# Optimization experiments

Hardware: AMD Instinct MI355X
Metric: run time of the kernel (lower is better)

The kernel has to match this reference:

```python
import jax, jax.numpy as jnp
import numpy as np

BATCH, SIZE_IN, SIZE_OUT = 2048, 256, 512


def setup_inputs() -> dict:
    key = jax.random.key(0)
    kx, ka = jax.random.split(key)
    x = jax.random.normal(kx, (BATCH, SIZE_IN), dtype=jnp.float32)
    A = jax.random.normal(ka, (SIZE_IN, SIZE_OUT), dtype=jnp.float32)
    return {"x": x, "A": A}


def reference(x, A):
    # W = sigmoid(A): [size_in, size_out]
    W = jax.nn.sigmoid(A)
    # tropical (max-times) matmul: out[i,k] = max_j W[j,k] * x[i,j]
    # broadcast [B,1,J_in->axis1]... x: [B,J,1], W: [1,J,K] -> [B,J,K] -> max over J
    out = jnp.max(x[:, :, None] * W[None, :, :], axis=1)  # [B, K]
    return out
```

## Files before the change

kernel.cpp:

```cpp
#include <hip/hip_runtime.h>


constexpr int JD = 256;
constexpr int KD = 512;
constexpr int TI = 4;
constexpr int ROWS = 16;
constexpr int NCH = 16;

typedef _Float16 h1;
typedef __attribute__((ext_vector_type(2))) _Float16 h2v;
typedef __attribute__((ext_vector_type(4))) float f4;

__device__ __forceinline__ float sigmoidf_fast(float a) {
    return 1.0f / (1.0f + __expf(-a));
}

__global__ __launch_bounds__(256) void wpack(const float* __restrict__ A,
                                             h2v* __restrict__ Wp) {
    const int t  = blockIdx.x * 256 + threadIdx.x;
    const int p  = t >> 7;
    const int kq = (t & 127) << 2;
    const f4 a0 = *(const f4*)&A[(2 * p) * KD + kq];
    const f4 a1 = *(const f4*)&A[(2 * p + 1) * KD + kq];
    union { f4 v; h2v h[4]; } u;
    #pragma unroll
    for (int q = 0; q < 4; ++q)
        u.h[q] = h2v{(h1)sigmoidf_fast(a0[q]), (h1)sigmoidf_fast(a1[q])};
    *(f4*)&Wp[p * KD + kq] = u.v;
}

__global__ __launch_bounds__(256, 4) void tropical_mm_kernel(
        const float* __restrict__ x,
        const h2v* __restrict__ Wp,
        float* __restrict__ out) {
    __shared__ h2v xl[ROWS][JD / 2];

    const int t    = (int)threadIdx.x;
    const int lane = t & 63;
    const int wv   = __builtin_amdgcn_readfirstlane(t >> 6);
    const int bk   = (int)blockIdx.x & 7;
    const int bi   = (int)blockIdx.x >> 3;
    const int i0   = bi * ROWS;
    const int k    = bk * 64 + lane;

    {
        const int srow = t >> 4;
        const int scf  = (t & 15) * 16;
        const float* xs = x + (i0 + srow) * JD + scf;
        f4 f0 = ((const f4*)xs)[0];
        f4 f1 = ((const f4*)xs)[1];
        f4 f2 = ((const f4*)xs)[2];
        f4 f3 = ((const f4*)xs)[3];
        union { f4 v; h2v h[4]; } u0, u1;
        u0.h[0] = h2v{(h1)f0.x, (h1)f0.y};
        u0.h[1] = h2v{(h1)f0.z, (h1)f0.w};
        u0.h[2] = h2v{(h1)f1.x, (h1)f1.y};
        u0.h[3] = h2v{(h1)f1.z, (h1)f1.w};
        u1.h[0] = h2v{(h1)f2.x, (h1)f2.y};
        u1.h[1] = h2v{(h1)f2.z, (h1)f2.w};
        u1.h[2] = h2v{(h1)f3.x, (h1)f3.y};
        u1.h[3] = h2v{(h1)f3.z, (h1)f3.w};
        *(f4*)&xl[srow][(t & 15) * 8]     = u0.v;
        *(f4*)&xl[srow][(t & 15) * 8 + 4] = u1.v;
    }
    __syncthreads();

    const h2v* Wk = Wp + k;
    const int r0 = wv * TI;

    h2v acc[TI];
    #pragma unroll
    for (int r = 0; r < TI; ++r)
        acc[r] = h2v{(h1)(-65504.0f), (h1)(-65504.0f)};

    h2v WA[8], WB[8];
    f4  XA[TI][2], XB[TI][2];

    auto loadW = [&](h2v (&W)[8], int c) {
        const h2v* p = Wk + (c * 8) * KD;
        #pragma unroll
        for (int q = 0; q < 8; ++q) W[q] = p[q * KD];
    };
    auto loadX = [&](f4 (&X)[TI][2], int c) {
        #pragma unroll
        for (int r = 0; r < TI; ++r) {
            X[r][0] = *(const f4*)&xl[r0 + r][c * 8];
            X[r][1] = *(const f4*)&xl[r0 + r][c * 8 + 4];
        }
    };
    auto compute = [&](const f4 (&X)[TI][2], const h2v (&W)[8]) {
        #pragma unroll
        for (int r = 0; r < TI; ++r) {
            #pragma unroll
            for (int hf = 0; hf < 2; ++hf) {
                union { f4 v; h2v h[4]; } u;
                u.v = X[r][hf];
                #pragma unroll
                for (int q = 0; q < 4; ++q)
                    acc[r] = __builtin_elementwise_max(
                        acc[r], u.h[q] * W[hf * 4 + q]);
            }
        }
    };

    loadW(WA, 0);
    loadX(XA, 0);

    #pragma unroll 1
    for (int c = 0; c < NCH; c += 2) {
        loadW(WB, c + 1);
        loadX(XB, c + 1);
        compute(XA, WA);
        if (c + 2 < NCH) {
            loadW(WA, c + 2);
            loadX(XA, c + 2);
        }
        compute(XB, WB);
    }

    #pragma unroll
    for (int r = 0; r < TI; ++r) {
        const float lo = (float)acc[r][0];
        const float hi = (float)acc[r][1];
        out[(i0 + r0 + r) * KD + k] = fmaxf(lo, hi);
    }
}

extern "C" void kernel_launch(void* const* d_in, const int* in_sizes, int n_in,
                              void* d_out, int out_size, void* d_ws, size_t ws_size,
                              hipStream_t stream) {
    const float* x = (const float*)d_in[0];
    const float* A = (const float*)d_in[1];
    float* out = (float*)d_out;
    h2v* Wp = (h2v*)d_ws;

    hipLaunchKernelGGL(wpack, dim3(64), dim3(256), 0, stream, A, Wp);

    hipLaunchKernelGGL(tropical_mm_kernel, dim3(1024), dim3(256), 0, stream,
                       x, Wp, out);
}
```

Measured before the change: 23.57 us.

## Fuse sigmoid packing into tropical matmul with W staged in LDS

```diff
diff --git a/kernel.cpp b/kernel.cpp
--- a/kernel.cpp
+++ b/kernel.cpp
@@ -1,129 +1,136 @@
 #include <hip/hip_runtime.h>
 
-
-constexpr int JD = 256;
-constexpr int KD = 512;
-constexpr int TI = 4;
-constexpr int ROWS = 16;
-constexpr int NCH = 16;
 
 typedef _Float16 h1;
 typedef __attribute__((ext_vector_type(2))) _Float16 h2v;
 typedef __attribute__((ext_vector_type(4))) float f4;
 
+constexpr int JD   = 256;
+constexpr int KD   = 512;
+constexpr int BI   = 32;
+constexpr int KW   = 64;
+constexpr int TI   = 8;
+constexpr int LSTR = 132;
+constexpr int NCH  = 16;
+
 __device__ __forceinline__ float sigmoidf_fast(float a) {
     return 1.0f / (1.0f + __expf(-a));
 }
 
-__global__ __launch_bounds__(256) void wpack(const float* __restrict__ A,
-                                             h2v* __restrict__ Wp) {
-    const int t  = blockIdx.x * 256 + threadIdx.x;
-    const int p  = t >> 7;
-    const int kq = (t & 127) << 2;
-    const f4 a0 = *(const f4*)&A[(2 * p) * KD + kq];
-    const f4 a1 = *(const f4*)&A[(2 * p + 1) * KD + kq];
-    union { f4 v; h2v h[4]; } u;
-    #pragma unroll
-    for (int q = 0; q < 4; ++q)
-        u.h[q] = h2v{(h1)sigmoidf_fast(a0[q]), (h1)sigmoidf_fast(a1[q])};
-    *(f4*)&Wp[p * KD + kq] = u.v;
-}
+__global__ __launch_bounds__(256) void tropical_fused(
+        const float* __restrict__ x,
+        const float* __restrict__ A,
+        float* __restrict__ out) {
+    __shared__ h2v xl[BI * LSTR];
+    __shared__ h2v Wl[KW * LSTR];
 
-__global__ __launch_bounds__(256, 4) void tropical_mm_kernel(
-        const float* __restrict__ x,
-        const h2v* __restrict__ Wp,
-        float* __restrict__ out) {
-    __shared__ h2v xl[ROWS][JD / 2];
-
-    const int t    = (int)threadIdx.x;
-    const int lane = t & 63;
-    const int wv   = __builtin_amdgcn_readfirstlane(t >> 6);
-    const int bk   = (int)blockIdx.x & 7;
-    const int bi   = (int)blockIdx.x >> 3;
-    const int i0   = bi * ROWS;
-    const int k    = bk * 64 + lane;
+    const int t  = (int)threadIdx.x;
+    const int kg = (int)blockIdx.x & 7;
+    const int ib = (int)blockIdx.x >> 3;
+    const int i0 = ib * BI;
+    const int k0 = kg * KW;
 
     {
-        const int srow = t >> 4;
-        const int scf  = (t & 15) * 16;
-        const float* xs = x + (i0 + srow) * JD + scf;
-        f4 f0 = ((const f4*)xs)[0];
-        f4 f1 = ((const f4*)xs)[1];
-        f4 f2 = ((const f4*)xs)[2];
-        f4 f3 = ((const f4*)xs)[3];
-        union { f4 v; h2v h[4]; } u0, u1;
-        u0.h[0] = h2v{(h1)f0.x, (h1)f0.y};
-        u0.h[1] = h2v{(h1)f0.z, (h1)f0.w};
-        u0.h[2] = h2v{(h1)f1.x, (h1)f1.y};
-        u0.h[3] = h2v{(h1)f1.z, (h1)f1.w};
-        u1.h[0] = h2v{(h1)f2.x, (h1)f2.y};
-        u1.h[1] = h2v{(h1)f2.z, (h1)f2.w};
-        u1.h[2] = h2v{(h1)f3.x, (h1)f3.y};
-        u1.h[3] = h2v{(h1)f3.z, (h1)f3.w};
-        *(f4*)&xl[srow][(t & 15) * 8]     = u0.v;
-        *(f4*)&xl[srow][(t & 15) * 8 + 4] = u1.v;
+        const int srow = t >> 3;
+        const int c0   = (t & 7) * 32;
+        const float* xs = x + (i0 + srow) * JD + c0;
+        #pragma unroll
+        for (int q = 0; q < 4; ++q) {
+            const f4 v0 = ((const f4*)xs)[2 * q];
+            const f4 v1 = ((const f4*)xs)[2 * q + 1];
+            union { f4 v; h2v h[4]; } u;
+            u.h[0] = h2v{(h1)v0.x, (h1)v0.y};
+            u.h[1] = h2v{(h1)v0.z, (h1)v0.w};
+            u.h[2] = h2v{(h1)v1.x, (h1)v1.y};
+            u.h[3] = h2v{(h1)v1.z, (h1)v1.w};
+            *(f4*)&xl[srow * LSTR + c0 / 2 + q * 4] = u.v;
+        }
+    }
+
+    {
+        const int kl = t & 63;
+        const int j0 = (t >> 6) * 64;
+        const float* Ak = A + k0 + kl;
+        #pragma unroll 1
+        for (int pass = 0; pass < 4; ++pass) {
+            const int jb = j0 + pass * 16;
+            float s[16];
+            #pragma unroll
+            for (int m = 0; m < 16; ++m)
+                s[m] = Ak[(jb + m) * KD];
+            union { f4 v; h2v h[4]; } u0, u1;
+            #pragma unroll
+            for (int m = 0; m < 4; ++m)
+                u0.h[m] = h2v{(h1)sigmoidf_fast(s[2 * m]),
+                              (h1)sigmoidf_fast(s[2 * m + 1])};
+            #pragma unroll
+            for (int m = 0; m < 4; ++m)
+                u1.h[m] = h2v{(h1)sigmoidf_fast(s[8 + 2 * m]),
+                              (h1)sigmoidf_fast(s[9 + 2 * m])};
+            *(f4*)&Wl[kl * LSTR + jb / 2]     = u0.v;
+            *(f4*)&Wl[kl * LSTR + jb / 2 + 4] = u1.v;
+        }
     }
     __syncthreads();
 
-    const h2v* Wk = Wp + k;
-    const int r0 = wv * TI;
+    const int lane = t & 63;
+    const int wv   = __builtin_amdgcn_readfirstlane(t >> 6);
+    const int r0   = wv * TI;
 
     h2v acc[TI];
     #pragma unroll
     for (int r = 0; r < TI; ++r)
         acc[r] = h2v{(h1)(-65504.0f), (h1)(-65504.0f)};
 
-    h2v WA[8], WB[8];
-    f4  XA[TI][2], XB[TI][2];
+    f4 XA[TI][2], XB[TI][2];
+    f4 WA[2], WB[2];
 
-    auto loadW = [&](h2v (&W)[8], int c) {
-        const h2v* p = Wk + (c * 8) * KD;
-        #pragma unroll
-        for (int q = 0; q < 8; ++q) W[q] = p[q * KD];
-    };
     auto loadX = [&](f4 (&X)[TI][2], int c) {
         #pragma unroll
         for (int r = 0; r < TI; ++r) {
-            X[r][0] = *(const f4*)&xl[r0 + r][c * 8];
-            X[r][1] = *(const f4*)&xl[r0 + r][c * 8 + 4];
+            X[r][0] = *(const f4*)&xl[(r0 + r) * LSTR + c * 8];
+            X[r][1] = *(const f4*)&xl[(r0 + r) * LSTR + c * 8 + 4];
         }
     };
-    auto compute = [&](const f4 (&X)[TI][2], const h2v (&W)[8]) {
+    auto loadW = [&](f4 (&W)[2], int c) {
+        W[0] = *(const f4*)&Wl[lane * LSTR + c * 8];
+        W[1] = *(const f4*)&Wl[lane * LSTR + c * 8 + 4];
+    };
+    auto compute = [&](const f4 (&X)[TI][2], const f4 (&W)[2]) {
         #pragma unroll
         for (int r = 0; r < TI; ++r) {
             #pragma unroll
             for (int hf = 0; hf < 2; ++hf) {
-                union { f4 v; h2v h[4]; } u;
-                u.v = X[r][hf];
+                union { f4 v; h2v h[4]; } ux, uw;
+                ux.v = X[r][hf];
+                uw.v = W[hf];
                 #pragma unroll
                 for (int q = 0; q < 4; ++q)
-                    acc[r] = __builtin_elementwise_max(
-                        acc[r], u.h[q] * W[hf * 4 + q]);
+                    acc[r] = __builtin_elementwise_max(acc[r],
+                                                       ux.h[q] * uw.h[q]);
             }
         }
     };
 
+    loadX(XA, 0);
     loadW(WA, 0);
-    loadX(XA, 0);
 
     #pragma unroll 1
     for (int c = 0; c < NCH; c += 2) {
+        loadX(XB, c + 1);
         loadW(WB, c + 1);
-        loadX(XB, c + 1);
         compute(XA, WA);
         if (c + 2 < NCH) {
+            loadX(XA, c + 2);
             loadW(WA, c + 2);
-            loadX(XA, c + 2);
         }
         compute(XB, WB);
     }
 
     #pragma unroll
-    for (int r = 0; r < TI; ++r) {
-        const float lo = (float)acc[r][0];
-        const float hi = (float)acc[r][1];
-        out[(i0 + r0 + r) * KD + k] = fmaxf(lo, hi);
-    }
+    for (int r = 0; r < TI; ++r)
+        out[(i0 + r0 + r) * KD + k0 + lane] =
+            fmaxf((float)acc[r][0], (float)acc[r][1]);
 }
 
 extern "C" void kernel_launch(void* const* d_in, const int* in_sizes, int n_in,
@@ -132,10 +139,7 @@
     const float* x = (const float*)d_in[0];
     const float* A = (const float*)d_in[1];
     float* out = (float*)d_out;
-    h2v* Wp = (h2v*)d_ws;
 
-    hipLaunchKernelGGL(wpack, dim3(64), dim3(256), 0, stream, A, Wp);
-
-    hipLaunchKernelGGL(tropical_mm_kernel, dim3(1024), dim3(256), 0, stream,
-                       x, Wp, out);
+    hipLaunchKernelGGL(tropical_fused, dim3(512), dim3(256), 0, stream,
+                       x, A, out);
 }
```

Result: no change. 23.15 us (-1.8%).
